# Performance work log

Hardware: AMD Instinct MI355X
Metric: run time of the kernel (lower is better)

Reference implementation:

```python
import jax, jax.numpy as jnp
import numpy as np

B, S, IN, D, H, L, F = 4, 1024, 6, 512, 8, 4, 2048
DK = D // H
EPS = 1e-5

def _pos_encoding(S, D):
    pos = np.arange(S, dtype=np.float32)[:, None]
    div = np.exp(np.arange(0, D, 2, dtype=np.float32) * (-np.log(10000.0) / D))
    pe = np.zeros((S, D), np.float32)
    pe[:, 0::2] = np.sin(pos * div)
    pe[:, 1::2] = np.cos(pos * div)
    return jnp.asarray(pe)

def setup_inputs() -> dict:
    key = jax.random.key(0)
    ks = jax.random.split(key, 12)
    def w(k, shape):
        return jax.random.normal(k, shape, jnp.float32) * 0.02
    return {
        "left_wrist": jax.random.normal(ks[0], (B, S, IN), jnp.float32),
        "right_wrist": jax.random.normal(ks[1], (B, S, IN), jnp.float32),
        "Wl": w(ks[2], (IN, D)), "bl": jnp.zeros((D,), jnp.float32),
        "Wr": w(ks[3], (IN, D)), "br": jnp.zeros((D,), jnp.float32),
        "pe": _pos_encoding(S, D),
        # 4 attention blocks per layer (cross1to2, cross2to1, self1, self2), each with q/k/v/o projections
        "mha_w": w(ks[4], (L, 4, 4, D, D)), "mha_b": jnp.zeros((L, 4, 4, D), jnp.float32),
        "mha_ln_g": jnp.ones((L, 4, D), jnp.float32), "mha_ln_b": jnp.zeros((L, 4, D), jnp.float32),
        # 2 FFNs per layer (channel 1 / channel 2)
        "ff_w1": w(ks[5], (L, 2, D, F)), "ff_b1": jnp.zeros((L, 2, F), jnp.float32),
        "ff_w2": w(ks[6], (L, 2, F, D)), "ff_b2": jnp.zeros((L, 2, D), jnp.float32),
        "ff_ln_g": jnp.ones((L, 2, D), jnp.float32), "ff_ln_b": jnp.zeros((L, 2, D), jnp.float32),
        "h1_w1": w(ks[7], (2 * D, D)), "h1_b1": jnp.zeros((D,), jnp.float32),
        "h1_w2": w(ks[8], (D, 2)), "h1_b2": jnp.zeros((2,), jnp.float32),
        "h2_w1": w(ks[9], (2 * D, D)), "h2_b1": jnp.zeros((D,), jnp.float32),
        "h2_w2": w(ks[10], (D, 2)), "h2_b2": jnp.zeros((2,), jnp.float32),
    }

def _ln(x, g, b):
    m = jnp.mean(x, axis=-1, keepdims=True)
    v = jnp.var(x, axis=-1, keepdims=True)
    return (x - m) * jax.lax.rsqrt(v + EPS) * g + b

def _mha(q_in, k_in, v_in, w, b, g, beta):
    # w: [4, D, D] for q/k/v/o, b: [4, D]
    def proj(x, i):
        return (x @ w[i] + b[i]).reshape(x.shape[0], x.shape[1], H, DK).transpose(0, 2, 1, 3)
    Q, K, V = proj(q_in, 0), proj(k_in, 1), proj(v_in, 2)
    scores = jnp.einsum('bhqd,bhkd->bhqk', Q, K) * np.float32(1.0 / np.sqrt(DK))
    attn = jax.nn.softmax(scores, axis=-1)
    ctx = jnp.einsum('bhqk,bhkd->bhqd', attn, V)
    ctx = ctx.transpose(0, 2, 1, 3).reshape(q_in.shape[0], q_in.shape[1], D)
    out = ctx @ w[3] + b[3]
    return _ln(out + q_in, g, beta)

def _ffn(x, w1, b1, w2, b2, g, beta):
    h = jax.nn.relu(x @ w1 + b1)
    return _ln(h @ w2 + b2 + x, g, beta)

def reference(left_wrist, right_wrist, Wl, bl, Wr, br, pe,
              mha_w, mha_b, mha_ln_g, mha_ln_b,
              ff_w1, ff_b1, ff_w2, ff_b2, ff_ln_g, ff_ln_b,
              h1_w1, h1_b1, h1_w2, h1_b2, h2_w1, h2_b1, h2_w2, h2_b2):
    left = left_wrist @ Wl + bl + pe[None]
    right = right_wrist @ Wr + br + pe[None]
    for l in range(L):
        lc = _mha(left, right, right, mha_w[l, 0], mha_b[l, 0], mha_ln_g[l, 0], mha_ln_b[l, 0])
        rc = _mha(right, left, left, mha_w[l, 1], mha_b[l, 1], mha_ln_g[l, 1], mha_ln_b[l, 1])
        ls = _mha(lc, lc, lc, mha_w[l, 2], mha_b[l, 2], mha_ln_g[l, 2], mha_ln_b[l, 2])
        rs = _mha(rc, rc, rc, mha_w[l, 3], mha_b[l, 3], mha_ln_g[l, 3], mha_ln_b[l, 3])
        left = _ffn(ls, ff_w1[l, 0], ff_b1[l, 0], ff_w2[l, 0], ff_b2[l, 0], ff_ln_g[l, 0], ff_ln_b[l, 0])
        right = _ffn(rs, ff_w1[l, 1], ff_b1[l, 1], ff_w2[l, 1], ff_b2[l, 1], ff_ln_g[l, 1], ff_ln_b[l, 1])
    # AdaptiveAvgPool1d(1) over seq == mean over seq axis
    fused = jnp.concatenate([jnp.mean(left, axis=1), jnp.mean(right, axis=1)], axis=1)  # [B, 2D]
    logits1 = jax.nn.relu(fused @ h1_w1 + h1_b1) @ h1_w2 + h1_b2
    logits2 = jax.nn.relu(fused @ h2_w1 + h2_b1) @ h2_w2 + h2_b2
    return (logits1, logits2)
```

## Files before the change

### kernel.cpp

```cpp
#include <hip/hip_runtime.h>
#include <hip/hip_bf16.h>

#define NB 4
#define NS 1024
#define NIN 6
#define ND 512
#define NH 8
#define NLAYERS 4
#define NF 2048
#define NDK 64
#define LN_EPS 1e-5f

typedef unsigned short u16;
typedef __attribute__((ext_vector_type(4))) unsigned short u16x4;
typedef __attribute__((ext_vector_type(8))) short s16x8;
typedef __attribute__((ext_vector_type(4))) float f32x4;
typedef __attribute__((ext_vector_type(4))) unsigned int u32x4;

#define MFMA_BF16(A, B, C) __builtin_amdgcn_mfma_f32_16x16x32_bf16(A, B, C, 0, 0, 0)

#define GLOAD_LDS16(gsrc, ldst)                                                  \
    __builtin_amdgcn_global_load_lds(                                            \
        (const __attribute__((address_space(1))) void*)(gsrc),                   \
        (__attribute__((address_space(3))) void*)(ldst), 16, 0, 0)

__device__ inline u16 f2bf(float f) {
    unsigned int u = __builtin_bit_cast(unsigned int, f);
    u += 0x7fffu + ((u >> 16) & 1u);
    return (u16)(u >> 16);
}

__global__ __launch_bounds__(256) void transpose_kernel(
    const float* __restrict__ src, u16* __restrict__ dst, int K, int N) {
    __shared__ u16 t[64][72];
    const int tid = threadIdx.x;
    src += (size_t)blockIdx.z * K * N;
    dst += (size_t)blockIdx.z * K * N;
    const int n0 = blockIdx.x * 64, k0 = blockIdx.y * 64;
    {
        int r = tid >> 2, cq = (tid & 3) * 16;
        const float* sp = src + (size_t)(k0 + r) * N + n0 + cq;
#pragma unroll
        for (int q = 0; q < 4; ++q) {
            float4 v = *reinterpret_cast<const float4*>(sp + q * 4);
            t[r][cq + q * 4 + 0] = f2bf(v.x);
            t[r][cq + q * 4 + 1] = f2bf(v.y);
            t[r][cq + q * 4 + 2] = f2bf(v.z);
            t[r][cq + q * 4 + 3] = f2bf(v.w);
        }
    }
    __syncthreads();
    {
        int rn = tid >> 2, cq = (tid & 3) * 16;
        s16x8 o0, o1;
#pragma unroll
        for (int j = 0; j < 8; ++j) o0[j] = (short)t[cq + j][rn];
#pragma unroll
        for (int j = 0; j < 8; ++j) o1[j] = (short)t[cq + 8 + j][rn];
        u16* dp = dst + (size_t)(n0 + rn) * K + k0 + cq;
        *reinterpret_cast<s16x8*>(dp) = o0;
        *reinterpret_cast<s16x8*>(dp + 8) = o1;
    }
}

__global__ __launch_bounds__(256) void in_proj_kernel(
    const float* __restrict__ x, const float* __restrict__ W,
    const float* __restrict__ bias, const float* __restrict__ pe,
    float* __restrict__ out, u16* __restrict__ outb) {
    int idx = blockIdx.x * 256 + threadIdx.x;
    int d = idx & (ND - 1);
    int bs = idx / ND;
    int s = bs & (NS - 1);
    const float* xr = x + (size_t)bs * NIN;
    float acc = bias[d] + pe[(size_t)s * ND + d];
#pragma unroll
    for (int i = 0; i < NIN; ++i) acc += xr[i] * W[(size_t)i * ND + d];
    out[idx] = acc;
    outb[idx] = f2bf(acc);
}

template <int BN>
__device__ inline void gemm_core(const u16* __restrict__ A, const u16* __restrict__ Wt,
                                 int K, int bm, int bn, char* lds, int tid,
                                 f32x4 (&acc)[4][BN / 32]) {
    constexpr int NT = BN / 32;
    constexpr int ASZ = 128 * 128;
    constexpr int BSZ = BN * 128;
    const int wid = tid >> 6, lane = tid & 63;
    const int l15 = lane & 15, lhi = lane >> 4;
    const int wr = wid >> 1, wc = wid & 1;

    auto stage = [&](int buf, int k0) {
#pragma unroll
        for (int i = 0; i < 4; ++i) {
            int slot = (wid * 4 + i) * 64 + lane;
            int r = slot >> 3, p = slot & 7;
            const char* src = (const char*)(A + (size_t)(bm + r) * K + k0)
                              + ((p * 16) ^ ((r & 7) << 4));
            GLOAD_LDS16(src, lds + buf * ASZ + (wid * 4 + i) * 1024);
        }
#pragma unroll
        for (int i = 0; i < BN / 32; ++i) {
            int slot = (wid * (BN / 32) + i) * 64 + lane;
            int r = slot >> 3, p = slot & 7;
            const char* src = (const char*)(Wt + (size_t)(bn + r) * K + k0)
                              + ((p * 16) ^ ((r & 7) << 4));
            GLOAD_LDS16(src, lds + 2 * ASZ + buf * BSZ + (wid * (BN / 32) + i) * 1024);
        }
    };

#pragma unroll
    for (int mt = 0; mt < 4; ++mt)
#pragma unroll
        for (int nt = 0; nt < NT; ++nt) acc[mt][nt] = f32x4{0.f, 0.f, 0.f, 0.f};

    const int KT = K >> 6;
    stage(0, 0);
    __syncthreads();
    for (int t = 0; t < KT; ++t) {
        if (t + 1 < KT) stage((t + 1) & 1, (t + 1) << 6);
        const char* Ab = lds + (t & 1) * ASZ;
        const char* Bb = lds + 2 * ASZ + (t & 1) * BSZ;
#pragma unroll
        for (int sl = 0; sl < 2; ++sl) {
            s16x8 af[4];
#pragma unroll
            for (int mt = 0; mt < 4; ++mt) {
                int row = wr * 64 + mt * 16 + l15;
                af[mt] = *reinterpret_cast<const s16x8*>(
                    Ab + ((row * 128 + sl * 64 + lhi * 16) ^ ((row & 7) << 4)));
            }
            s16x8 bfr[NT];
#pragma unroll
            for (int nt = 0; nt < NT; ++nt) {
                int row = wc * (BN / 2) + nt * 16 + l15;
                bfr[nt] = *reinterpret_cast<const s16x8*>(
                    Bb + ((row * 128 + sl * 64 + lhi * 16) ^ ((row & 7) << 4)));
            }
#pragma unroll
            for (int mt = 0; mt < 4; ++mt)
#pragma unroll
                for (int nt = 0; nt < NT; ++nt)
                    acc[mt][nt] = MFMA_BF16(af[mt], bfr[nt], acc[mt][nt]);
        }
        __syncthreads();
    }
}

template <int OMODE, int BN>
__global__ __launch_bounds__(256) void bgemm2_kernel(
    const u16* __restrict__ a0, const u16* __restrict__ a1,
    const u16* __restrict__ wt0, const u16* __restrict__ wt1,
    const float* __restrict__ bias0, const float* __restrict__ bias1,
    void* __restrict__ Cv, int M, int N, int K) {
    constexpr int NT = BN / 32;
    __shared__ char lds[2 * 128 * 128 + 2 * BN * 128];
    const int tid = threadIdx.x, z = blockIdx.z;
    const int bm = blockIdx.y * 128, bn = blockIdx.x * BN;
    const u16* A = z ? a1 : a0;
    const u16* Wt = z ? wt1 : wt0;
    const float* bias = z ? bias1 : bias0;

    f32x4 acc[4][NT];
    gemm_core<BN>(A, Wt, K, bm, bn, lds, tid, acc);

    const int wid = tid >> 6, lane = tid & 63;
    const int l15 = lane & 15, lhi = lane >> 4;
    const int wr = wid >> 1, wc = wid & 1;
    float bv[NT];
#pragma unroll
    for (int nt = 0; nt < NT; ++nt) bv[nt] = bias[bn + wc * (BN / 2) + nt * 16 + l15];

    if (OMODE == 0) {
        float* C = (float*)Cv + (size_t)z * M * N;
#pragma unroll
        for (int mt = 0; mt < 4; ++mt) {
            int m0 = bm + wr * 64 + mt * 16 + lhi * 4;
#pragma unroll
            for (int nt = 0; nt < NT; ++nt) {
                int n = bn + wc * (BN / 2) + nt * 16 + l15;
#pragma unroll
                for (int r = 0; r < 4; ++r)
                    C[(size_t)(m0 + r) * N + n] = acc[mt][nt][r] + bv[nt];
            }
        }
    } else {
        u16* C = (u16*)Cv + (size_t)z * M * N;
#pragma unroll
        for (int mt = 0; mt < 4; ++mt) {
            int m0 = bm + wr * 64 + mt * 16 + lhi * 4;
#pragma unroll
            for (int nt = 0; nt < NT; ++nt) {
                int n = bn + wc * (BN / 2) + nt * 16 + l15;
#pragma unroll
                for (int r = 0; r < 4; ++r) {
                    float v = acc[mt][nt][r] + bv[nt];
                    if (OMODE == 1) v = fmaxf(v, 0.f);
                    C[(size_t)(m0 + r) * N + n] = f2bf(v);
                }
            }
        }
    }
}

__global__ __launch_bounds__(256) void bgemm_qkv_kernel(
    const u16* __restrict__ aq0, const u16* __restrict__ aq1,
    const u16* __restrict__ akv0, const u16* __restrict__ akv1,
    const u16* __restrict__ wt0, const u16* __restrict__ wt1,
    const float* __restrict__ bb0, const float* __restrict__ bb1,
    u16* __restrict__ Qo, u16* __restrict__ Ko, u16* __restrict__ Vto) {
    __shared__ char lds[2 * 128 * 128 + 2 * 64 * 128];
    const int tid = threadIdx.x, z = blockIdx.z;
    const int proj = blockIdx.x >> 3;
    const int bm = blockIdx.y * 128, bn = (blockIdx.x & 7) * 64;
    const int M = NB * NS;
    const u16* A = (proj == 0) ? (z ? aq1 : aq0) : (z ? akv1 : akv0);
    const u16* Wt = (z ? wt1 : wt0) + (size_t)proj * ND * ND;
    const float* bias = (z ? bb1 : bb0) + proj * ND;

    f32x4 acc[4][2];
    gemm_core<64>(A, Wt, ND, bm, bn, lds, tid, acc);

    const int wid = tid >> 6, lane = tid & 63;
    const int l15 = lane & 15, lhi = lane >> 4;
    const int wr = wid >> 1, wc = wid & 1;
    float bv[2];
#pragma unroll
    for (int nt = 0; nt < 2; ++nt) bv[nt] = bias[bn + wc * 32 + nt * 16 + l15];

    if (proj < 2) {
        u16* C = (proj ? Ko : Qo) + (size_t)z * M * ND;
#pragma unroll
        for (int mt = 0; mt < 4; ++mt) {
            int m0 = bm + wr * 64 + mt * 16 + lhi * 4;
#pragma unroll
            for (int nt = 0; nt < 2; ++nt) {
                int n = bn + wc * 32 + nt * 16 + l15;
#pragma unroll
                for (int r = 0; r < 4; ++r)
                    C[(size_t)(m0 + r) * ND + n] = f2bf(acc[mt][nt][r] + bv[nt]);
            }
        }
    } else {
#pragma unroll
        for (int mt = 0; mt < 4; ++mt) {
            int m0 = bm + wr * 64 + mt * 16 + lhi * 4;
            int b = (z * M + m0) >> 10, s = m0 & (NS - 1);
#pragma unroll
            for (int nt = 0; nt < 2; ++nt) {
                int n = bn + wc * 32 + nt * 16 + l15;
                int h = n >> 6, dk = n & 63;
                u16x4 o = {f2bf(acc[mt][nt][0] + bv[nt]), f2bf(acc[mt][nt][1] + bv[nt]),
                           f2bf(acc[mt][nt][2] + bv[nt]), f2bf(acc[mt][nt][3] + bv[nt])};
                *reinterpret_cast<u16x4*>(Vto + ((size_t)((b * NH + h) * NDK + dk)) * NS + s) = o;
            }
        }
    }
}

__global__ __launch_bounds__(256) void ln2_kernel(
    const float* __restrict__ x, const float* __restrict__ res,
    const float* __restrict__ g0, const float* __restrict__ g1,
    const float* __restrict__ be0, const float* __restrict__ be1,
    float* __restrict__ outf, u16* __restrict__ outb) {
    int row = blockIdx.x;
    const float* g = (row >> 12) ? g1 : g0;
    const float* be = (row >> 12) ? be1 : be0;
    int tid = threadIdx.x;
    const float* xr = x + (size_t)row * ND;
    const float* rr = res + (size_t)row * ND;
    float v0 = xr[tid] + rr[tid];
    float v1 = xr[tid + 256] + rr[tid + 256];
    float s = v0 + v1, sq = v0 * v0 + v1 * v1;
#pragma unroll
    for (int m = 1; m < 64; m <<= 1) { s += __shfl_xor(s, m); sq += __shfl_xor(sq, m); }
    __shared__ float ls[4], lq[4];
    int wid = tid >> 6, lane = tid & 63;
    if (lane == 0) { ls[wid] = s; lq[wid] = sq; }
    __syncthreads();
    s = ls[0] + ls[1] + ls[2] + ls[3];
    sq = lq[0] + lq[1] + lq[2] + lq[3];
    float mean = s * (1.f / ND);
    float var = sq * (1.f / ND) - mean * mean;
    float rstd = rsqrtf(var + LN_EPS);
    float o0 = (v0 - mean) * rstd * g[tid] + be[tid];
    float o1 = (v1 - mean) * rstd * g[tid + 256] + be[tid + 256];
    outf[(size_t)row * ND + tid] = o0;
    outf[(size_t)row * ND + tid + 256] = o1;
    outb[(size_t)row * ND + tid] = f2bf(o0);
    outb[(size_t)row * ND + tid + 256] = f2bf(o1);
}

__global__ __launch_bounds__(256) void attn_kernel(
    const u16* __restrict__ Qb, const u16* __restrict__ Kb,
    const u16* __restrict__ Vtb, u16* __restrict__ O) {
    __shared__ u16 Ks[64 * 64];
    __shared__ u16 Vts[64 * 64];
    __shared__ u16 Ps[4][16 * 64];

    const int tid = threadIdx.x;
    const int w = tid >> 6, lane = tid & 63;
    const int l15 = lane & 15, lhi = lane >> 4;
    const int bh = blockIdx.y;
    const int b = bh >> 3, h = bh & 7;
    const int qb = blockIdx.x * 64 + w * 16;

    s16x8 qf[2];
    {
        const u16* qp = Qb + ((size_t)(b * NS) + qb + l15) * ND + h * NDK + lhi * 8;
        qf[0] = *reinterpret_cast<const s16x8*>(qp);
        qf[1] = *reinterpret_cast<const s16x8*>(qp + 32);
    }

    f32x4 o[4] = {f32x4{0.f, 0.f, 0.f, 0.f}, f32x4{0.f, 0.f, 0.f, 0.f},
                  f32x4{0.f, 0.f, 0.f, 0.f}, f32x4{0.f, 0.f, 0.f, 0.f}};
    float m[4] = {-1e30f, -1e30f, -1e30f, -1e30f};
    float lsum[4] = {0.f, 0.f, 0.f, 0.f};

    const u16* Kbase = Kb + ((size_t)(b * NS)) * ND + h * NDK;
    const u16* Vbase = Vtb + ((size_t)bh * NDK) * NS;

    for (int c = 0; c < NS / 64; ++c) {
        const int kv0 = c * 64;
        __syncthreads();
#pragma unroll
        for (int ss = 0; ss < 2; ++ss) {
            int s = tid + ss * 256;
            int r = s >> 3, c8 = s & 7;
            u32x4 kv = *reinterpret_cast<const u32x4*>(
                Kbase + (size_t)(kv0 + r) * ND + c8 * 8);
            *reinterpret_cast<u32x4*>((char*)Ks +
                ((r * 128 + c8 * 16) ^ ((r & 7) << 4))) = kv;
            u32x4 vv = *reinterpret_cast<const u32x4*>(
                Vbase + (size_t)r * NS + kv0 + c8 * 8);
            *reinterpret_cast<u32x4*>((char*)Vts +
                ((r * 128 + c8 * 16) ^ ((r & 7) << 4))) = vv;
        }
        __syncthreads();

        f32x4 sc[4] = {f32x4{0.f, 0.f, 0.f, 0.f}, f32x4{0.f, 0.f, 0.f, 0.f},
                       f32x4{0.f, 0.f, 0.f, 0.f}, f32x4{0.f, 0.f, 0.f, 0.f}};
#pragma unroll
        for (int sl = 0; sl < 2; ++sl) {
#pragma unroll
            for (int kb = 0; kb < 4; ++kb) {
                int krow = kb * 16 + l15;
                s16x8 kf = *reinterpret_cast<const s16x8*>((char*)Ks +
                    ((krow * 128 + sl * 64 + lhi * 16) ^ ((krow & 7) << 4)));
                sc[kb] = MFMA_BF16(qf[sl], kf, sc[kb]);
            }
        }
        float corr[4];
#pragma unroll
        for (int r = 0; r < 4; ++r) {
            float s0 = sc[0][r] * 0.125f, s1 = sc[1][r] * 0.125f;
            float s2 = sc[2][r] * 0.125f, s3 = sc[3][r] * 0.125f;
            float mx = fmaxf(fmaxf(s0, s1), fmaxf(s2, s3));
#pragma unroll
            for (int msk = 1; msk < 16; msk <<= 1) mx = fmaxf(mx, __shfl_xor(mx, msk));
            float mn = fmaxf(m[r], mx);
            corr[r] = __expf(m[r] - mn);
            m[r] = mn;
            float p0 = __expf(s0 - mn), p1 = __expf(s1 - mn);
            float p2 = __expf(s2 - mn), p3 = __expf(s3 - mn);
            sc[0][r] = p0; sc[1][r] = p1; sc[2][r] = p2; sc[3][r] = p3;
            float rs = p0 + p1 + p2 + p3;
#pragma unroll
            for (int msk = 1; msk < 16; msk <<= 1) rs += __shfl_xor(rs, msk);
            lsum[r] = lsum[r] * corr[r] + rs;
        }
#pragma unroll
        for (int r = 0; r < 4; ++r) {
            int row = lhi * 4 + r;
#pragma unroll
            for (int kb = 0; kb < 4; ++kb) {
                int col = kb * 16 + l15;
                *reinterpret_cast<u16*>((char*)(Ps[w]) +
                    ((row * 128 + col * 2) ^ ((row & 7) << 4))) = f2bf(sc[kb][r]);
            }
        }
#pragma unroll
        for (int db = 0; db < 4; ++db)
#pragma unroll
            for (int r = 0; r < 4; ++r) o[db][r] *= corr[r];
        s16x8 pf[2];
#pragma unroll
        for (int sl = 0; sl < 2; ++sl)
            pf[sl] = *reinterpret_cast<const s16x8*>((char*)(Ps[w]) +
                ((l15 * 128 + sl * 64 + lhi * 16) ^ ((l15 & 7) << 4)));
#pragma unroll
        for (int sl = 0; sl < 2; ++sl) {
#pragma unroll
            for (int db = 0; db < 4; ++db) {
                int vr = db * 16 + l15;
                s16x8 vf = *reinterpret_cast<const s16x8*>((char*)Vts +
                    ((vr * 128 + sl * 64 + lhi * 16) ^ ((vr & 7) << 4)));
                o[db] = MFMA_BF16(pf[sl], vf, o[db]);
            }
        }
    }
#pragma unroll
    for (int db = 0; db < 4; ++db) {
#pragma unroll
        for (int r = 0; r < 4; ++r) {
            int q = qb + lhi * 4 + r;
            O[((size_t)(b * NS) + q) * ND + h * NDK + db * 16 + l15] =
                f2bf(o[db][r] / lsum[r]);
        }
    }
}

__global__ __launch_bounds__(256) void pool_kernel(
    const float* __restrict__ Lb, const float* __restrict__ Rb,
    float* __restrict__ fused) {
    int idx = blockIdx.x * 256 + threadIdx.x;
    int b = idx >> 10;
    int c = idx & 1023;
    const float* src = (c < ND) ? (Lb + ((size_t)b * NS) * ND + c)
                                : (Rb + ((size_t)b * NS) * ND + (c - ND));
    float s = 0.f;
    for (int t = 0; t < NS; ++t) s += src[(size_t)t * ND];
    fused[idx] = s * (1.f / NS);
}

__global__ __launch_bounds__(256) void head_hidden_kernel(
    const float* __restrict__ fused,
    const float* __restrict__ w1a, const float* __restrict__ b1a,
    const float* __restrict__ w1b, const float* __restrict__ b1b,
    float* __restrict__ hid) {
    const int b = blockIdx.x >> 1, head = blockIdx.x & 1;
    const float* w1 = head ? w1b : w1a;
    const float* b1 = head ? b1b : b1a;
    const int tid = threadIdx.x;
    const int j = blockIdx.y * 64 + (tid & 63);
    const int kq = tid >> 6;
    const float* fr = fused + (size_t)b * (2 * ND);
    float p = 0.f;
    for (int k = kq * 256; k < kq * 256 + 256; ++k)
        p += fr[k] * w1[(size_t)k * ND + j];
    __shared__ float part[4][64];
    part[kq][tid & 63] = p;
    __syncthreads();
    if (tid < 64) {
        float v = part[0][tid] + part[1][tid] + part[2][tid] + part[3][tid] + b1[j];
        hid[(size_t)blockIdx.x * ND + j] = fmaxf(v, 0.f);
    }
}

__global__ __launch_bounds__(256) void head_out_kernel(
    const float* __restrict__ hid,
    const float* __restrict__ w2a, const float* __restrict__ b2a,
    const float* __restrict__ w2b, const float* __restrict__ b2b,
    float* __restrict__ out) {
    const int b = blockIdx.x >> 1, head = blockIdx.x & 1;
    const float* w2 = head ? w2b : w2a;
    const float* b2 = head ? b2b : b2a;
    const int tid = threadIdx.x;
    const float* hr = hid + (size_t)blockIdx.x * ND;
    float h0 = hr[tid], h1 = hr[tid + 256];
    float p0 = h0 * w2[tid * 2 + 0] + h1 * w2[(tid + 256) * 2 + 0];
    float p1 = h0 * w2[tid * 2 + 1] + h1 * w2[(tid + 256) * 2 + 1];
#pragma unroll
    for (int m = 1; m < 64; m <<= 1) { p0 += __shfl_xor(p0, m); p1 += __shfl_xor(p1, m); }
    __shared__ float r0s[4], r1s[4];
    int wid = tid >> 6, lane = tid & 63;
    if (lane == 0) { r0s[wid] = p0; r1s[wid] = p1; }
    __syncthreads();
    if (tid == 0) {
        out[head * 8 + b * 2 + 0] = r0s[0] + r0s[1] + r0s[2] + r0s[3] + b2[0];
        out[head * 8 + b * 2 + 1] = r1s[0] + r1s[1] + r1s[2] + r1s[3] + b2[1];
    }
}

extern "C" void kernel_launch(void* const* d_in, const int* in_sizes, int n_in,
                              void* d_out, int out_size, void* d_ws, size_t ws_size,
                              hipStream_t stream) {
    const float* left_wrist  = (const float*)d_in[0];
    const float* right_wrist = (const float*)d_in[1];
    const float* Wl = (const float*)d_in[2];
    const float* bl = (const float*)d_in[3];
    const float* Wr = (const float*)d_in[4];
    const float* br = (const float*)d_in[5];
    const float* pe = (const float*)d_in[6];
    const float* mha_w    = (const float*)d_in[7];
    const float* mha_b    = (const float*)d_in[8];
    const float* mha_ln_g = (const float*)d_in[9];
    const float* mha_ln_b = (const float*)d_in[10];
    const float* ff_w1 = (const float*)d_in[11];
    const float* ff_b1 = (const float*)d_in[12];
    const float* ff_w2 = (const float*)d_in[13];
    const float* ff_b2 = (const float*)d_in[14];
    const float* ff_ln_g = (const float*)d_in[15];
    const float* ff_ln_b = (const float*)d_in[16];
    const float* h1_w1 = (const float*)d_in[17];
    const float* h1_b1 = (const float*)d_in[18];
    const float* h1_w2 = (const float*)d_in[19];
    const float* h1_b2 = (const float*)d_in[20];
    const float* h2_w1 = (const float*)d_in[21];
    const float* h2_b1 = (const float*)d_in[22];
    const float* h2_w2 = (const float*)d_in[23];
    const float* h2_b2 = (const float*)d_in[24];
    float* out = (float*)d_out;

    const size_t NTOK = (size_t)NB * NS * ND;
    const int M = NB * NS;
    float* ws = (float*)d_ws;
    float* RES   = ws;
    float* CRES  = RES + 2 * NTOK;
    float* TMPf  = CRES + 2 * NTOK;
    float* FUSED = TMPf + 2 * NTOK;
    float* HID   = FUSED + NB * 2 * ND;
    u16* Xbf  = (u16*)(HID + 8 * ND);
    u16* CXbf = Xbf + 2 * NTOK;
    u16* Qbf  = CXbf + 2 * NTOK;
    u16* Kbf  = Qbf + 2 * NTOK;
    u16* Vtbf = Kbf + 2 * NTOK;
    u16* CTbf = Vtbf + 2 * NTOK;
    u16* Hh   = Qbf;
    u16* WtM  = CTbf + 2 * NTOK;
    u16* WtF1 = WtM + (size_t)64 * ND * ND;
    u16* WtF2 = WtF1 + (size_t)8 * ND * NF;

    const size_t DD = (size_t)ND * ND;

    transpose_kernel<<<dim3(ND / 64, ND / 64, 64), 256, 0, stream>>>(mha_w, WtM, ND, ND);
    transpose_kernel<<<dim3(NF / 64, ND / 64, 8), 256, 0, stream>>>(ff_w1, WtF1, ND, NF);
    transpose_kernel<<<dim3(ND / 64, NF / 64, 8), 256, 0, stream>>>(ff_w2, WtF2, NF, ND);

    in_proj_kernel<<<(NB * NS * ND) / 256, 256, 0, stream>>>(left_wrist, Wl, bl, pe, RES, Xbf);
    in_proj_kernel<<<(NB * NS * ND) / 256, 256, 0, stream>>>(right_wrist, Wr, br, pe,
                                                             RES + NTOK, Xbf + NTOK);

    for (int l = 0; l < NLAYERS; ++l) {
        const u16* wt0 = WtM + ((size_t)l * 4 + 0) * 4 * DD;
        const u16* wt1 = WtM + ((size_t)l * 4 + 1) * 4 * DD;
        const u16* wt2 = WtM + ((size_t)l * 4 + 2) * 4 * DD;
        const u16* wt3 = WtM + ((size_t)l * 4 + 3) * 4 * DD;
        const float* bb0 = mha_b + ((size_t)l * 4 + 0) * 4 * ND;
        const float* bb1 = mha_b + ((size_t)l * 4 + 1) * 4 * ND;
        const float* bb2 = mha_b + ((size_t)l * 4 + 2) * 4 * ND;
        const float* bb3 = mha_b + ((size_t)l * 4 + 3) * 4 * ND;

        bgemm_qkv_kernel<<<dim3(24, 32, 2), 256, 0, stream>>>(
            Xbf, Xbf + NTOK, Xbf + NTOK, Xbf, wt0, wt1, bb0, bb1, Qbf, Kbf, Vtbf);
        attn_kernel<<<dim3(NS / 64, 2 * NB * NH), 256, 0, stream>>>(Qbf, Kbf, Vtbf, CTbf);
        bgemm2_kernel<0, 64><<<dim3(8, 32, 2), 256, 0, stream>>>(
            CTbf, CTbf + NTOK, wt0 + 3 * DD, wt1 + 3 * DD, bb0 + 3 * ND, bb1 + 3 * ND,
            TMPf, M, ND, ND);
        ln2_kernel<<<2 * M, 256, 0, stream>>>(
            TMPf, RES, mha_ln_g + ((size_t)l * 4 + 0) * ND, mha_ln_g + ((size_t)l * 4 + 1) * ND,
            mha_ln_b + ((size_t)l * 4 + 0) * ND, mha_ln_b + ((size_t)l * 4 + 1) * ND,
            CRES, CXbf);

        bgemm_qkv_kernel<<<dim3(24, 32, 2), 256, 0, stream>>>(
            CXbf, CXbf + NTOK, CXbf, CXbf + NTOK, wt2, wt3, bb2, bb3, Qbf, Kbf, Vtbf);
        attn_kernel<<<dim3(NS / 64, 2 * NB * NH), 256, 0, stream>>>(Qbf, Kbf, Vtbf, CTbf);
        bgemm2_kernel<0, 64><<<dim3(8, 32, 2), 256, 0, stream>>>(
            CTbf, CTbf + NTOK, wt2 + 3 * DD, wt3 + 3 * DD, bb2 + 3 * ND, bb3 + 3 * ND,
            TMPf, M, ND, ND);
        ln2_kernel<<<2 * M, 256, 0, stream>>>(
            TMPf, CRES, mha_ln_g + ((size_t)l * 4 + 2) * ND, mha_ln_g + ((size_t)l * 4 + 3) * ND,
            mha_ln_b + ((size_t)l * 4 + 2) * ND, mha_ln_b + ((size_t)l * 4 + 3) * ND,
            RES, Xbf);

        bgemm2_kernel<1, 128><<<dim3(16, 32, 2), 256, 0, stream>>>(
            Xbf, Xbf + NTOK, WtF1 + ((size_t)l * 2 + 0) * ND * NF, WtF1 + ((size_t)l * 2 + 1) * ND * NF,
            ff_b1 + ((size_t)l * 2 + 0) * NF, ff_b1 + ((size_t)l * 2 + 1) * NF,
            Hh, M, NF, ND);
        bgemm2_kernel<0, 64><<<dim3(8, 32, 2), 256, 0, stream>>>(
            Hh, Hh + (size_t)M * NF, WtF2 + ((size_t)l * 2 + 0) * NF * ND, WtF2 + ((size_t)l * 2 + 1) * NF * ND,
            ff_b2 + ((size_t)l * 2 + 0) * ND, ff_b2 + ((size_t)l * 2 + 1) * ND,
            TMPf, M, ND, NF);
        ln2_kernel<<<2 * M, 256, 0, stream>>>(
            TMPf, RES, ff_ln_g + ((size_t)l * 2 + 0) * ND, ff_ln_g + ((size_t)l * 2 + 1) * ND,
            ff_ln_b + ((size_t)l * 2 + 0) * ND, ff_ln_b + ((size_t)l * 2 + 1) * ND,
            RES, Xbf);
    }

    pool_kernel<<<(NB * 2 * ND) / 256, 256, 0, stream>>>(RES, RES + NTOK, FUSED);
    head_hidden_kernel<<<dim3(8, 8), 256, 0, stream>>>(FUSED, h1_w1, h1_b1, h2_w1, h2_b1, HID);
    head_out_kernel<<<8, 256, 0, stream>>>(HID, h1_w2, h1_b2, h2_w2, h2_b2, out);
}
```

Baseline: 1.480 ms.

## Widen attention KV tiles to 128 with transposed score MFMA and split pooling

Attention now stages 128 keys per iteration instead of 64, which halves the number of barriers and online-softmax rescales. The QK^T MFMA operands are swapped so each lane holds one query's scores, cutting the row max and sum reductions to two shuffles. P is then written packed to LDS, and the per-row correction factors are broadcast with shuffles. The final mean-pool is split across 8 sequence chunks with atomicAdd into a zeroed buffer, exposing more parallelism; this adds a memset launch and makes the float summation order non-deterministic.

```diff
diff --git a/kernel.cpp b/kernel.cpp
--- a/kernel.cpp
+++ b/kernel.cpp
@@ -294,9 +294,9 @@
 __global__ __launch_bounds__(256) void attn_kernel(
     const u16* __restrict__ Qb, const u16* __restrict__ Kb,
     const u16* __restrict__ Vtb, u16* __restrict__ O) {
-    __shared__ u16 Ks[64 * 64];
-    __shared__ u16 Vts[64 * 64];
-    __shared__ u16 Ps[4][16 * 64];
+    __shared__ u16 Ks[128 * 64];
+    __shared__ u16 Vts[64 * 128];
+    __shared__ u16 Ps[4][16 * 128];
 
     const int tid = threadIdx.x;
     const int w = tid >> 6, lane = tid & 63;
@@ -314,113 +314,130 @@
 
     f32x4 o[4] = {f32x4{0.f, 0.f, 0.f, 0.f}, f32x4{0.f, 0.f, 0.f, 0.f},
                   f32x4{0.f, 0.f, 0.f, 0.f}, f32x4{0.f, 0.f, 0.f, 0.f}};
-    float m[4] = {-1e30f, -1e30f, -1e30f, -1e30f};
-    float lsum[4] = {0.f, 0.f, 0.f, 0.f};
+    float m = -1e30f;
+    float lsum = 0.f;
 
     const u16* Kbase = Kb + ((size_t)(b * NS)) * ND + h * NDK;
     const u16* Vbase = Vtb + ((size_t)bh * NDK) * NS;
 
-    for (int c = 0; c < NS / 64; ++c) {
-        const int kv0 = c * 64;
+    for (int c = 0; c < NS / 128; ++c) {
+        const int kv0 = c * 128;
         __syncthreads();
 #pragma unroll
-        for (int ss = 0; ss < 2; ++ss) {
-            int s = tid + ss * 256;
-            int r = s >> 3, c8 = s & 7;
-            u32x4 kv = *reinterpret_cast<const u32x4*>(
-                Kbase + (size_t)(kv0 + r) * ND + c8 * 8);
-            *reinterpret_cast<u32x4*>((char*)Ks +
-                ((r * 128 + c8 * 16) ^ ((r & 7) << 4))) = kv;
-            u32x4 vv = *reinterpret_cast<const u32x4*>(
-                Vbase + (size_t)r * NS + kv0 + c8 * 8);
-            *reinterpret_cast<u32x4*>((char*)Vts +
-                ((r * 128 + c8 * 16) ^ ((r & 7) << 4))) = vv;
+        for (int i = 0; i < 4; ++i) {
+            int s = i * 256 + tid;
+            {
+                int r = s >> 3, p = s & 7;
+                u32x4 kv = *reinterpret_cast<const u32x4*>(
+                    Kbase + (size_t)(kv0 + r) * ND + p * 8);
+                *reinterpret_cast<u32x4*>((char*)Ks +
+                    ((r * 128 + p * 16) ^ ((r & 7) << 4))) = kv;
+            }
+            {
+                int r = s >> 4, p = s & 15;
+                u32x4 vv = *reinterpret_cast<const u32x4*>(
+                    Vbase + (size_t)r * NS + kv0 + p * 8);
+                *reinterpret_cast<u32x4*>((char*)Vts +
+                    ((r * 256 + p * 16) ^ ((r & 7) << 4))) = vv;
+            }
         }
         __syncthreads();
 
-        f32x4 sc[4] = {f32x4{0.f, 0.f, 0.f, 0.f}, f32x4{0.f, 0.f, 0.f, 0.f},
-                       f32x4{0.f, 0.f, 0.f, 0.f}, f32x4{0.f, 0.f, 0.f, 0.f}};
+        f32x4 sc[8];
+#pragma unroll
+        for (int blk = 0; blk < 8; ++blk) sc[blk] = f32x4{0.f, 0.f, 0.f, 0.f};
 #pragma unroll
         for (int sl = 0; sl < 2; ++sl) {
 #pragma unroll
-            for (int kb = 0; kb < 4; ++kb) {
-                int krow = kb * 16 + l15;
+            for (int blk = 0; blk < 8; ++blk) {
+                int krow = blk * 16 + l15;
                 s16x8 kf = *reinterpret_cast<const s16x8*>((char*)Ks +
                     ((krow * 128 + sl * 64 + lhi * 16) ^ ((krow & 7) << 4)));
-                sc[kb] = MFMA_BF16(qf[sl], kf, sc[kb]);
-            }
-        }
-        float corr[4];
-#pragma unroll
-        for (int r = 0; r < 4; ++r) {
-            float s0 = sc[0][r] * 0.125f, s1 = sc[1][r] * 0.125f;
-            float s2 = sc[2][r] * 0.125f, s3 = sc[3][r] * 0.125f;
-            float mx = fmaxf(fmaxf(s0, s1), fmaxf(s2, s3));
-#pragma unroll
-            for (int msk = 1; msk < 16; msk <<= 1) mx = fmaxf(mx, __shfl_xor(mx, msk));
-            float mn = fmaxf(m[r], mx);
-            corr[r] = __expf(m[r] - mn);
-            m[r] = mn;
-            float p0 = __expf(s0 - mn), p1 = __expf(s1 - mn);
-            float p2 = __expf(s2 - mn), p3 = __expf(s3 - mn);
-            sc[0][r] = p0; sc[1][r] = p1; sc[2][r] = p2; sc[3][r] = p3;
-            float rs = p0 + p1 + p2 + p3;
-#pragma unroll
-            for (int msk = 1; msk < 16; msk <<= 1) rs += __shfl_xor(rs, msk);
-            lsum[r] = lsum[r] * corr[r] + rs;
-        }
-#pragma unroll
-        for (int r = 0; r < 4; ++r) {
-            int row = lhi * 4 + r;
-#pragma unroll
-            for (int kb = 0; kb < 4; ++kb) {
-                int col = kb * 16 + l15;
-                *reinterpret_cast<u16*>((char*)(Ps[w]) +
-                    ((row * 128 + col * 2) ^ ((row & 7) << 4))) = f2bf(sc[kb][r]);
-            }
-        }
+                sc[blk] = MFMA_BF16(kf, qf[sl], sc[blk]);
+            }
+        }
+        float mx = -1e30f;
+#pragma unroll
+        for (int blk = 0; blk < 8; ++blk) {
+#pragma unroll
+            for (int r = 0; r < 4; ++r) {
+                float v = sc[blk][r] * 0.125f;
+                sc[blk][r] = v;
+                mx = fmaxf(mx, v);
+            }
+        }
+        mx = fmaxf(mx, __shfl_xor(mx, 16));
+        mx = fmaxf(mx, __shfl_xor(mx, 32));
+        float mn = fmaxf(m, mx);
+        float corr = __expf(m - mn);
+        m = mn;
+        float rs = 0.f;
+#pragma unroll
+        for (int blk = 0; blk < 8; ++blk) {
+#pragma unroll
+            for (int r = 0; r < 4; ++r) {
+                float p = __expf(sc[blk][r] - mn);
+                sc[blk][r] = p;
+                rs += p;
+            }
+        }
+        rs += __shfl_xor(rs, 16);
+        rs += __shfl_xor(rs, 32);
+        lsum = lsum * corr + rs;
+#pragma unroll
+        for (int blk = 0; blk < 8; ++blk) {
+            u16x4 pk = {f2bf(sc[blk][0]), f2bf(sc[blk][1]),
+                        f2bf(sc[blk][2]), f2bf(sc[blk][3])};
+            *reinterpret_cast<u16x4*>((char*)(Ps[w]) +
+                ((l15 * 256 + blk * 32 + lhi * 8) ^ ((l15 & 7) << 4))) = pk;
+        }
+        float cO[4];
+#pragma unroll
+        for (int r = 0; r < 4; ++r) cO[r] = __shfl(corr, lhi * 4 + r);
 #pragma unroll
         for (int db = 0; db < 4; ++db)
 #pragma unroll
-            for (int r = 0; r < 4; ++r) o[db][r] *= corr[r];
-        s16x8 pf[2];
-#pragma unroll
-        for (int sl = 0; sl < 2; ++sl)
-            pf[sl] = *reinterpret_cast<const s16x8*>((char*)(Ps[w]) +
-                ((l15 * 128 + sl * 64 + lhi * 16) ^ ((l15 & 7) << 4)));
-#pragma unroll
-        for (int sl = 0; sl < 2; ++sl) {
+            for (int r = 0; r < 4; ++r) o[db][r] *= cO[r];
+#pragma unroll
+        for (int sl2 = 0; sl2 < 4; ++sl2) {
+            s16x8 pf = *reinterpret_cast<const s16x8*>((char*)(Ps[w]) +
+                ((l15 * 256 + sl2 * 64 + lhi * 16) ^ ((l15 & 7) << 4)));
 #pragma unroll
             for (int db = 0; db < 4; ++db) {
                 int vr = db * 16 + l15;
                 s16x8 vf = *reinterpret_cast<const s16x8*>((char*)Vts +
-                    ((vr * 128 + sl * 64 + lhi * 16) ^ ((vr & 7) << 4)));
-                o[db] = MFMA_BF16(pf[sl], vf, o[db]);
-            }
-        }
-    }
+                    ((vr * 256 + sl2 * 64 + lhi * 16) ^ ((vr & 7) << 4)));
+                o[db] = MFMA_BF16(pf, vf, o[db]);
+            }
+        }
+    }
+    float lsO[4];
+#pragma unroll
+    for (int r = 0; r < 4; ++r) lsO[r] = __shfl(lsum, lhi * 4 + r);
 #pragma unroll
     for (int db = 0; db < 4; ++db) {
 #pragma unroll
         for (int r = 0; r < 4; ++r) {
             int q = qb + lhi * 4 + r;
             O[((size_t)(b * NS) + q) * ND + h * NDK + db * 16 + l15] =
-                f2bf(o[db][r] / lsum[r]);
-        }
-    }
-}
-
-__global__ __launch_bounds__(256) void pool_kernel(
-    const float* __restrict__ Lb, const float* __restrict__ Rb,
-    float* __restrict__ fused) {
-    int idx = blockIdx.x * 256 + threadIdx.x;
-    int b = idx >> 10;
-    int c = idx & 1023;
-    const float* src = (c < ND) ? (Lb + ((size_t)b * NS) * ND + c)
-                                : (Rb + ((size_t)b * NS) * ND + (c - ND));
-    float s = 0.f;
-    for (int t = 0; t < NS; ++t) s += src[(size_t)t * ND];
-    fused[idx] = s * (1.f / NS);
+                f2bf(o[db][r] / lsO[r]);
+        }
+    }
+}
+
+__global__ __launch_bounds__(256) void pool2_kernel(
+    const float* __restrict__ RES, float* __restrict__ fused) {
+    const int b = blockIdx.x, half = blockIdx.y, sc = blockIdx.z;
+    const size_t NTOK = (size_t)NB * NS * ND;
+    const float* src = RES + (half ? NTOK : 0) + ((size_t)(b * NS + sc * 128)) * ND;
+    const int tid = threadIdx.x;
+#pragma unroll
+    for (int cc = 0; cc < 2; ++cc) {
+        int c = cc * 256 + tid;
+        float s = 0.f;
+        for (int r = 0; r < 128; ++r) s += src[(size_t)r * ND + c];
+        atomicAdd(&fused[b * 1024 + half * 512 + c], s * (1.f / NS));
+    }
 }
 
 __global__ __launch_bounds__(256) void head_hidden_kernel(
@@ -577,7 +594,8 @@
             RES, Xbf);
     }
 
-    pool_kernel<<<(NB * 2 * ND) / 256, 256, 0, stream>>>(RES, RES + NTOK, FUSED);
+    hipMemsetAsync(FUSED, 0, NB * 2 * ND * sizeof(float), stream);
+    pool2_kernel<<<dim3(NB, 2, 8), 256, 0, stream>>>(RES, FUSED);
     head_hidden_kernel<<<dim3(8, 8), 256, 0, stream>>>(FUSED, h1_w1, h1_b1, h2_w1, h2_b1, HID);
     head_out_kernel<<<8, 256, 0, stream>>>(HID, h1_w2, h1_b2, h2_w2, h2_b2, out);
 }
```

New measurement: 1.347 ms. 1.1x faster.
